# Kernel tuning notes

Hardware: AMD Instinct MI355X
Metric: run time of the kernel (lower is better)

Reference implementation:

```python
import jax, jax.numpy as jnp
import numpy as np

N_NODES = 50000
N_EDGES = 800000
F_IN = 128
HID = 32
HEADS = 8
N_CLS = 2
NEG_SLOPE = 0.2


def _segment_softmax(logits, seg, num_segments):
    # logits: [E, H], seg: [E] destination indices
    m = jax.ops.segment_max(logits, seg, num_segments=num_segments)  # [N, H]
    m = jnp.where(jnp.isfinite(m), m, 0.0)
    e = jnp.exp(logits - m[seg])
    s = jax.ops.segment_sum(e, seg, num_segments=num_segments)  # [N, H]
    return e / (s[seg] + 1e-16)


def _gat_conv(x, src, dst, W, a_src, a_dst, bias, heads, out_ch, concat):
    N = x.shape[0]
    h = (x @ W).reshape(N, heads, out_ch)           # [N, H, C]
    alpha_src = jnp.einsum('nhc,hc->nh', h, a_src)  # [N, H]
    alpha_dst = jnp.einsum('nhc,hc->nh', h, a_dst)  # [N, H]
    logits = jax.nn.leaky_relu(alpha_src[src] + alpha_dst[dst], NEG_SLOPE)  # [E, H]
    alpha = _segment_softmax(logits, dst, N)        # [E, H]
    msg = h[src] * alpha[:, :, None]                # [E, H, C]
    out = jax.ops.segment_sum(msg, dst, num_segments=N)  # [N, H, C]
    out = out.reshape(N, heads * out_ch) if concat else out.mean(axis=1)
    return out + bias


def setup_inputs() -> dict:
    key = jax.random.key(0)
    ks = jax.random.split(key, 12)
    x = jax.random.normal(ks[0], (N_NODES, F_IN), dtype=jnp.float32)
    edge_index = jax.random.randint(ks[1], (2, N_EDGES), 0, N_NODES, dtype=jnp.int32)
    batch = jnp.zeros((N_NODES,), dtype=jnp.int32)
    g1 = 1.0 / np.sqrt(F_IN)
    g2 = 1.0 / np.sqrt(HEADS * HID)
    W1 = jax.random.normal(ks[2], (F_IN, HEADS * HID), dtype=jnp.float32) * g1
    a1_src = jax.random.normal(ks[3], (HEADS, HID), dtype=jnp.float32) * g2
    a1_dst = jax.random.normal(ks[4], (HEADS, HID), dtype=jnp.float32) * g2
    b1 = jnp.zeros((HEADS * HID,), dtype=jnp.float32)
    W2 = jax.random.normal(ks[5], (HEADS * HID, N_CLS), dtype=jnp.float32) * g2
    a2_src = jax.random.normal(ks[6], (1, N_CLS), dtype=jnp.float32)
    a2_dst = jax.random.normal(ks[7], (1, N_CLS), dtype=jnp.float32)
    b2 = jnp.zeros((N_CLS,), dtype=jnp.float32)
    return {"x": x, "edge_index": edge_index, "batch": batch,
            "W1": W1, "a1_src": a1_src, "a1_dst": a1_dst, "b1": b1,
            "W2": W2, "a2_src": a2_src, "a2_dst": a2_dst, "b2": b2}


def reference(x, edge_index, batch, W1, a1_src, a1_dst, b1, W2, a2_src, a2_dst, b2):
    N = x.shape[0]
    # PyG GATConv default add_self_loops=True
    loops = jnp.arange(N, dtype=edge_index.dtype)
    src = jnp.concatenate([edge_index[0], loops])
    dst = jnp.concatenate([edge_index[1], loops])
    # dropout layers are no-ops at inference (training=False)
    h = _gat_conv(x, src, dst, W1, a1_src, a1_dst, b1, HEADS, HID, concat=True)
    h = jax.nn.elu(h)
    out = _gat_conv(h, src, dst, W2, a2_src, a2_dst, b2, 1, N_CLS, concat=False)
    return out
```

## Files before the change

### kernel.cpp

```cpp
#include <hip/hip_runtime.h>

#define NN 50000
#define NP 50048
#define NE 800000
#define ET (NE + NN)
#define NB 196
#define CAP 8192
#define EPB 4096
#define P1_B ((ET + EPB - 1) / EPB)
#define CONVW_B 32
#define CONVX_B 391
#define FRONT_B (P1_B + CONVW_B + CONVX_B)
#define GEMM_B (NP / 64)
#define MID_B (NB + GEMM_B)
#define AGG1_B 2048

typedef __attribute__((ext_vector_type(8))) short short8;
typedef __attribute__((ext_vector_type(4))) float f32x4;

static __device__ __forceinline__ float bf2f(unsigned short u) {
  union { unsigned int i; float f; } v; v.i = ((unsigned int)u) << 16; return v.f;
}
static __device__ __forceinline__ unsigned short f2bf(float f) {
  union { unsigned int i; float f; } v; v.f = f;
  unsigned int r = v.i + 0x7fffu + ((v.i >> 16) & 1u);
  return (unsigned short)(r >> 16);
}
static __device__ __forceinline__ float lrelu(float z) { return z > 0.f ? z : 0.2f * z; }

__global__ __launch_bounds__(1024) void k_front(
    const int* __restrict__ ei, int* __restrict__ gcount, int* __restrict__ tmp,
    const float* __restrict__ W1, unsigned short* __restrict__ wh,
    const float* __restrict__ x, unsigned short* __restrict__ xh) {
  __shared__ int hist[NB];
  __shared__ int lbase[NB];
  const int b = blockIdx.x;
  const int tid = threadIdx.x;
  if (b < P1_B) {
    if (tid < NB) hist[tid] = 0;
    __syncthreads();
    const int e0 = b * EPB + tid;
    int bkv[4], locv[4], pkv[4];
    bool val[4];
#pragma unroll
    for (int j = 0; j < 4; ++j) {
      int e = e0 + j * 1024;
      val[j] = (e < ET);
      int s = 0, d = 0;
      if (val[j]) {
        s = (e < NE) ? ei[e] : (e - NE);
        d = (e < NE) ? ei[NE + e] : (e - NE);
      }
      bkv[j] = d >> 8;
      pkv[j] = (s << 8) | (d & 255);
      locv[j] = val[j] ? atomicAdd(&hist[bkv[j]], 1) : 0;
    }
    __syncthreads();
    if (tid < NB) {
      int c = hist[tid];
      lbase[tid] = (c > 0) ? atomicAdd(&gcount[tid], c) : 0;
    }
    __syncthreads();
#pragma unroll
    for (int j = 0; j < 4; ++j)
      if (val[j]) tmp[bkv[j] * CAP + lbase[bkv[j]] + locv[j]] = pkv[j];
  } else if (b < P1_B + CONVW_B) {
    int i = (b - P1_B) * 1024 + tid;
    int k = i >> 8, n = i & 255;
    wh[n * 128 + k] = f2bf(W1[i]);
  } else {
    int base = (b - P1_B - CONVW_B) * 4096 + tid;
#pragma unroll
    for (int k = 0; k < 4; ++k) {
      int i4 = base + k * 1024;
      int i = i4 * 4;
      int row = i >> 7;
      float4 v = (row < NN) ? *(const float4*)(x + i) : (float4){0.f, 0.f, 0.f, 0.f};
      ushort4 h;
      h.x = f2bf(v.x);
      h.y = f2bf(v.y);
      h.z = f2bf(v.z);
      h.w = f2bf(v.w);
      *(ushort4*)(xh + i) = h;
    }
  }
}

__global__ __launch_bounds__(256) void k_mid(
    const int* __restrict__ tmp, const int* __restrict__ gcount,
    int* __restrict__ ssrc, int* __restrict__ row_ptr,
    const unsigned short* __restrict__ xh, const unsigned short* __restrict__ wh,
    const float* __restrict__ a1s, const float* __restrict__ a1d,
    unsigned short* __restrict__ h1, float* __restrict__ as1, float* __restrict__ ad1) {
  __shared__ unsigned short hst[64][264];
  const int tid = threadIdx.x;
  if (blockIdx.x < NB) {
    int* hist = (int*)&hst[0][0];
    int* sa = hist + 256;
    int* sb = sa + 256;
    int* cur = sb + 256;
    int* base_sh = cur + 256;
    const int t = tid;
    const int b = blockIdx.x;
    const int n_b = gcount[b];
    sa[t] = (t < NB) ? gcount[t] : 0;
    __syncthreads();
    {
      int* s = sa;
      int* d = sb;
      for (int off = 1; off < 256; off <<= 1) {
        int v = s[t];
        if (t >= off) v += s[t - off];
        d[t] = v;
        int* tm = s; s = d; d = tm;
        __syncthreads();
      }
      if (t == 0) {
        base_sh[0] = (b == 0) ? 0 : s[b - 1];
        if (b == 0) row_ptr[NN] = ET;
      }
    }
    hist[t] = 0;
    __syncthreads();
    const int base = base_sh[0];
    for (int i = t; i < n_b; i += 256) {
      int p = tmp[b * CAP + i];
      atomicAdd(&hist[p & 255], 1);
    }
    __syncthreads();
    sa[t] = hist[t];
    __syncthreads();
    {
      int* s = sa;
      int* d = sb;
      for (int off = 1; off < 256; off <<= 1) {
        int v = s[t];
        if (t >= off) v += s[t - off];
        d[t] = v;
        int* tm = s; s = d; d = tm;
        __syncthreads();
      }
      int excl = (t == 0) ? 0 : s[t - 1];
      int start = base + excl;
      cur[t] = start;
      int d_glob = (b << 8) + t;
      if (d_glob < NN) row_ptr[d_glob] = start;
    }
    __syncthreads();
    for (int i = t; i < n_b; i += 256) {
      int p = tmp[b * CAP + i];
      int pos = atomicAdd(&cur[p & 255], 1);
      ssrc[pos] = p >> 8;
    }
    return;
  }
  const int gb = blockIdx.x - NB;
  const int w = tid >> 6, lane = tid & 63;
  const int quad = lane >> 4, m16 = lane & 15;
  const int row0 = gb * 64;
  const int koff = quad * 8;

  f32x4 acc[4][4];
  for (int mt = 0; mt < 4; ++mt)
    for (int nt = 0; nt < 4; ++nt) acc[mt][nt] = (f32x4){0.f, 0.f, 0.f, 0.f};

  for (int kt = 0; kt < 4; ++kt) {
    short8 ah[4], bh[4];
    for (int mt = 0; mt < 4; ++mt) {
      size_t ra = (size_t)(row0 + mt * 16 + m16) * 128 + kt * 32 + koff;
      ah[mt] = *(const short8*)(xh + ra);
    }
    for (int nt = 0; nt < 4; ++nt) {
      size_t rb = (size_t)(w * 64 + nt * 16 + m16) * 128 + kt * 32 + koff;
      bh[nt] = *(const short8*)(wh + rb);
    }
    for (int mt = 0; mt < 4; ++mt)
      for (int nt = 0; nt < 4; ++nt)
        acc[mt][nt] = __builtin_amdgcn_mfma_f32_16x16x32_bf16(ah[mt], bh[nt], acc[mt][nt], 0, 0, 0);
  }
  for (int mt = 0; mt < 4; ++mt)
    for (int nt = 0; nt < 4; ++nt) {
      int c = w * 64 + nt * 16 + m16;
      int rb = mt * 16 + quad * 4;
      for (int r = 0; r < 4; ++r) hst[rb + r][c] = f2bf(acc[mt][nt][r]);
    }
  __syncthreads();
  for (int p = 0; p < 8; ++p) {
    int idx = p * 256 + tid;
    int row = idx >> 5, u4 = idx & 31;
    int grow = row0 + row;
    if (grow < NN) {
      uint4 v = *(const uint4*)&hst[row][u4 * 8];
      *(uint4*)(h1 + (size_t)grow * 256 + u4 * 8) = v;
    }
  }
  for (int p = 0; p < 2; ++p) {
    int id = p * 256 + tid;
    int row = id >> 3, head = id & 7;
    int grow = row0 + row;
    if (grow < NN) {
      float sa = 0.f, sd = 0.f;
      for (int c = 0; c < 32; ++c) {
        float hv = bf2f(hst[row][head * 32 + c]);
        sa = fmaf(hv, a1s[head * 32 + c], sa);
        sd = fmaf(hv, a1d[head * 32 + c], sd);
      }
      as1[(size_t)grow * 8 + head] = sa;
      ad1[(size_t)grow * 8 + head] = sd;
    }
  }
}

__global__ __launch_bounds__(256) void k_agg1(
    const int* __restrict__ row_ptr, const int* __restrict__ ssrc,
    const unsigned short* __restrict__ h1, const float* __restrict__ as1,
    const float* __restrict__ ad1, const float* __restrict__ b1,
    const float* __restrict__ W2, const float* __restrict__ a2s,
    const float* __restrict__ a2d, float4* __restrict__ nd) {
  const int lane = threadIdx.x & 63;
  const int hA = lane & 7;
  const int eoff = lane >> 3;
  const int hB = lane >> 3;
  const int cB = (lane & 7) * 4;
  for (int dst = (int)(blockIdx.x * 4 + (threadIdx.x >> 6)); dst < NN; dst += AGG1_B * 4) {
    const int start = row_ptr[dst], end = row_ptr[dst + 1];
    const float ad_h = ad1[(size_t)dst * 8 + hA];
    float s_loc = 0.f;
    float acc0 = 0.f, acc1 = 0.f, acc2 = 0.f, acc3 = 0.f;
    for (int base = start; base < end; base += 16) {
      int ea = base + eoff, eb = base + 8 + eoff;
      int sa_ = 0, sb_ = 0;
      float wa = 0.f, wb = 0.f;
      if (ea < end) {
        sa_ = ssrc[ea];
        wa = __expf(lrelu(as1[(size_t)sa_ * 8 + hA] + ad_h));
      }
      if (eb < end) {
        sb_ = ssrc[eb];
        wb = __expf(lrelu(as1[(size_t)sb_ * 8 + hA] + ad_h));
      }
      s_loc += wa + wb;
      uint2 u[16];
      float w16[16];
#pragma unroll
      for (int j = 0; j < 8; ++j) {
        int se = __shfl(sa_, j * 8);
        w16[j] = __shfl(wa, j * 8 + hB);
        u[j] = *(const uint2*)(h1 + (size_t)se * 256 + hB * 32 + cB);
      }
#pragma unroll
      for (int j = 0; j < 8; ++j) {
        int se = __shfl(sb_, j * 8);
        w16[8 + j] = __shfl(wb, j * 8 + hB);
        u[8 + j] = *(const uint2*)(h1 + (size_t)se * 256 + hB * 32 + cB);
      }
#pragma unroll
      for (int j = 0; j < 16; ++j) {
        float w = w16[j];
        acc0 = fmaf(w, bf2f((unsigned short)(u[j].x & 0xffffu)), acc0);
        acc1 = fmaf(w, bf2f((unsigned short)(u[j].x >> 16)), acc1);
        acc2 = fmaf(w, bf2f((unsigned short)(u[j].y & 0xffffu)), acc2);
        acc3 = fmaf(w, bf2f((unsigned short)(u[j].y >> 16)), acc3);
      }
    }
    float s_red = s_loc;
    s_red += __shfl_xor(s_red, 8);
    s_red += __shfl_xor(s_red, 16);
    s_red += __shfl_xor(s_red, 32);
    const float inv_s = 1.f / (s_red + 1e-16f);
    const float inv_sB = __shfl(inv_s, hB);
    float a0 = acc0 * inv_sB, a1 = acc1 * inv_sB, a2 = acc2 * inv_sB, a3 = acc3 * inv_sB;
    const int col = hB * 32 + cB;
    float av[4] = {a0, a1, a2, a3};
    float tp0 = 0.f, tp1 = 0.f;
    for (int j = 0; j < 4; ++j) {
      float v = av[j] + b1[col + j];
      v = v > 0.f ? v : (__expf(v) - 1.f);
      tp0 = fmaf(v, W2[(col + j) * 2 + 0], tp0);
      tp1 = fmaf(v, W2[(col + j) * 2 + 1], tp1);
    }
    for (int off = 32; off >= 1; off >>= 1) {
      tp0 += __shfl_xor(tp0, off);
      tp1 += __shfl_xor(tp1, off);
    }
    if (lane == 0) {
      float s2v = tp0 * a2s[0] + tp1 * a2s[1];
      float d2v = tp0 * a2d[0] + tp1 * a2d[1];
      nd[dst] = (float4){tp0, tp1, s2v, d2v};
    }
  }
}

__global__ __launch_bounds__(256) void k_agg2(
    const int* __restrict__ row_ptr, const int* __restrict__ ssrc,
    const float4* __restrict__ nd, const float* __restrict__ b2,
    float* __restrict__ out) {
  int gid = blockIdx.x * 256 + threadIdx.x;
  int n = gid >> 3;
  int l8 = threadIdx.x & 7;
  if (n >= NN) return;
  int st = row_ptr[n], en = row_ptr[n + 1];
  float dv = nd[n].w;
  float ssum = 0.f, o0 = 0.f, o1 = 0.f;
  for (int e = st + l8; e < en; e += 8) {
    int s = ssrc[e];
    float4 v = nd[s];
    float w = __expf(lrelu(v.z + dv));
    ssum += w;
    o0 = fmaf(w, v.x, o0);
    o1 = fmaf(w, v.y, o1);
  }
  ssum += __shfl_xor(ssum, 1); o0 += __shfl_xor(o0, 1); o1 += __shfl_xor(o1, 1);
  ssum += __shfl_xor(ssum, 2); o0 += __shfl_xor(o0, 2); o1 += __shfl_xor(o1, 2);
  ssum += __shfl_xor(ssum, 4); o0 += __shfl_xor(o0, 4); o1 += __shfl_xor(o1, 4);
  if (l8 == 0) {
    float inv = 1.f / (ssum + 1e-16f);
    out[(size_t)n * 2 + 0] = o0 * inv + b2[0];
    out[(size_t)n * 2 + 1] = o1 * inv + b2[1];
  }
}

extern "C" void kernel_launch(void* const* d_in, const int* in_sizes, int n_in,
                              void* d_out, int out_size, void* d_ws, size_t ws_size,
                              hipStream_t stream) {
  const float* x = (const float*)d_in[0];
  const int* ei = (const int*)d_in[1];
  const float* W1 = (const float*)d_in[3];
  const float* a1s = (const float*)d_in[4];
  const float* a1d = (const float*)d_in[5];
  const float* b1 = (const float*)d_in[6];
  const float* W2 = (const float*)d_in[7];
  const float* a2s = (const float*)d_in[8];
  const float* a2d = (const float*)d_in[9];
  const float* b2 = (const float*)d_in[10];
  float* out = (float*)d_out;

  char* ws = (char*)d_ws;
  size_t off = 0;
  auto alloc = [&](size_t bytes) -> void* {
    void* p = ws + off;
    off += (bytes + 255) & ~(size_t)255;
    return p;
  };
  int* gcount = (int*)alloc((size_t)NB * 4);
  int* tmp = (int*)alloc((size_t)NB * CAP * 4);
  int* row_ptr = (int*)alloc((size_t)(NN + 1) * 4);
  int* ssrc = (int*)alloc((size_t)ET * 4);
  unsigned short* xh = (unsigned short*)alloc((size_t)NP * 128 * 2);
  unsigned short* wh = (unsigned short*)alloc((size_t)32768 * 2);
  unsigned short* h1 = (unsigned short*)alloc((size_t)NN * 256 * 2);
  float* as1 = (float*)alloc((size_t)NN * 8 * 4);
  float* ad1 = (float*)alloc((size_t)NN * 8 * 4);
  float4* nd = (float4*)alloc((size_t)NN * 16);
  (void)ws_size; (void)in_sizes; (void)n_in; (void)out_size;

  hipMemsetAsync(gcount, 0, (size_t)NB * 4, stream);
  k_front<<<FRONT_B, 1024, 0, stream>>>(ei, gcount, tmp, W1, wh, x, xh);
  k_mid<<<MID_B, 256, 0, stream>>>(tmp, gcount, ssrc, row_ptr, xh, wh, a1s, a1d, h1, as1, ad1);
  k_agg1<<<AGG1_B, 256, 0, stream>>>(row_ptr, ssrc, h1, as1, ad1, b1, W2, a2s, a2d, nd);
  k_agg2<<<(NN * 8 + 255) / 256, 256, 0, stream>>>(row_ptr, ssrc, nd, b2, out);
}
```

Measured before the change: 213.8 us.

## Fuse all stages into one persistent kernel with global grid barriers

Replaces the four kernel launches with a single persistent kernel whose grid is sized from the occupancy query. Blocks loop over virtual work items in each phase and synchronize through an atomic global barrier, removing launch gaps and kernel-boundary drains. Work granularity shrinks to fit 256-thread blocks (GEMM tiles drop to 32 rows). The spin barrier relies on every block being co-resident and adds atomic polling cost at three phase boundaries.

```diff
diff --git a/kernel.cpp b/kernel.cpp
--- a/kernel.cpp
+++ b/kernel.cpp
@@ -6,14 +6,16 @@
 #define ET (NE + NN)
 #define NB 196
 #define CAP 8192
-#define EPB 4096
-#define P1_B ((ET + EPB - 1) / EPB)
-#define CONVW_B 32
-#define CONVX_B 391
-#define FRONT_B (P1_B + CONVW_B + CONVX_B)
-#define GEMM_B (NP / 64)
-#define MID_B (NB + GEMM_B)
-#define AGG1_B 2048
+
+#define P1V 831
+#define CWV 128
+#define CXV 1564
+#define PH1 (P1V + CWV + CXV)
+#define SORTV NB
+#define GEMMV 1564
+#define PH2 (SORTV + GEMMV)
+#define PH3 12500
+#define PH4 1563
 
 typedef __attribute__((ext_vector_type(8))) short short8;
 typedef __attribute__((ext_vector_type(4))) float f32x4;
@@ -28,295 +30,304 @@
 }
 static __device__ __forceinline__ float lrelu(float z) { return z > 0.f ? z : 0.2f * z; }
 
-__global__ __launch_bounds__(1024) void k_front(
-    const int* __restrict__ ei, int* __restrict__ gcount, int* __restrict__ tmp,
-    const float* __restrict__ W1, unsigned short* __restrict__ wh,
-    const float* __restrict__ x, unsigned short* __restrict__ xh) {
-  __shared__ int hist[NB];
-  __shared__ int lbase[NB];
-  const int b = blockIdx.x;
+static __device__ __forceinline__ void gbar(int* bar, int target) {
+  __syncthreads();
+  if (threadIdx.x == 0) {
+    __threadfence();
+    __hip_atomic_fetch_add(bar, 1, __ATOMIC_ACQ_REL, __HIP_MEMORY_SCOPE_AGENT);
+    while (__hip_atomic_load(bar, __ATOMIC_ACQUIRE, __HIP_MEMORY_SCOPE_AGENT) < target)
+      __builtin_amdgcn_s_sleep(2);
+    __threadfence();
+  }
+  __syncthreads();
+}
+
+__global__ __launch_bounds__(256) void k_fused(
+    int* __restrict__ bar, const int* __restrict__ ei, int* __restrict__ gcount,
+    int* __restrict__ tmp, const float* __restrict__ W1, unsigned short* __restrict__ wh,
+    const float* __restrict__ x, unsigned short* __restrict__ xh,
+    const float* __restrict__ a1s, const float* __restrict__ a1d,
+    int* __restrict__ ssrc, int* __restrict__ row_ptr,
+    unsigned short* __restrict__ h1, float* __restrict__ as1, float* __restrict__ ad1,
+    const float* __restrict__ b1, const float* __restrict__ W2,
+    const float* __restrict__ a2s, const float* __restrict__ a2d,
+    float4* __restrict__ nd, const float* __restrict__ b2, float* __restrict__ out) {
+  __shared__ __align__(16) char smraw[32 * 264 * 2];
   const int tid = threadIdx.x;
-  if (b < P1_B) {
-    if (tid < NB) hist[tid] = 0;
-    __syncthreads();
-    const int e0 = b * EPB + tid;
-    int bkv[4], locv[4], pkv[4];
-    bool val[4];
-#pragma unroll
-    for (int j = 0; j < 4; ++j) {
-      int e = e0 + j * 1024;
-      val[j] = (e < ET);
-      int s = 0, d = 0;
-      if (val[j]) {
-        s = (e < NE) ? ei[e] : (e - NE);
-        d = (e < NE) ? ei[NE + e] : (e - NE);
-      }
-      bkv[j] = d >> 8;
-      pkv[j] = (s << 8) | (d & 255);
-      locv[j] = val[j] ? atomicAdd(&hist[bkv[j]], 1) : 0;
+  const int G = (int)gridDim.x;
+
+  for (int v = blockIdx.x; v < PH1; v += G) {
+    if (v < P1V) {
+      int* hist = (int*)smraw;
+      int* lbase = hist + 256;
+      if (tid < NB) hist[tid] = 0;
+      __syncthreads();
+      int bkv[4], locv[4], pkv[4];
+      bool val[4];
+#pragma unroll
+      for (int j = 0; j < 4; ++j) {
+        int e = v * 1024 + tid + j * 256;
+        val[j] = (e < ET);
+        int s = 0, d = 0;
+        if (val[j]) {
+          s = (e < NE) ? ei[e] : (e - NE);
+          d = (e < NE) ? ei[NE + e] : (e - NE);
+        }
+        bkv[j] = d >> 8;
+        pkv[j] = (s << 8) | (d & 255);
+        locv[j] = val[j] ? atomicAdd(&hist[bkv[j]], 1) : 0;
+      }
+      __syncthreads();
+      if (tid < NB) {
+        int c = hist[tid];
+        lbase[tid] = (c > 0) ? atomicAdd(&gcount[tid], c) : 0;
+      }
+      __syncthreads();
+#pragma unroll
+      for (int j = 0; j < 4; ++j)
+        if (val[j]) tmp[bkv[j] * CAP + lbase[bkv[j]] + locv[j]] = pkv[j];
+      __syncthreads();
+    } else if (v < P1V + CWV) {
+      int i = (v - P1V) * 256 + tid;
+      int k = i >> 8, n = i & 255;
+      wh[n * 128 + k] = f2bf(W1[i]);
+    } else {
+      int base = (v - P1V - CWV) * 1024 + tid;
+#pragma unroll
+      for (int j = 0; j < 4; ++j) {
+        int i4 = base + j * 256;
+        int i = i4 * 4;
+        int row = i >> 7;
+        float4 vv = (row < NN) ? *(const float4*)(x + i) : (float4){0.f, 0.f, 0.f, 0.f};
+        ushort4 h;
+        h.x = f2bf(vv.x); h.y = f2bf(vv.y); h.z = f2bf(vv.z); h.w = f2bf(vv.w);
+        *(ushort4*)(xh + i) = h;
+      }
     }
-    __syncthreads();
-    if (tid < NB) {
-      int c = hist[tid];
-      lbase[tid] = (c > 0) ? atomicAdd(&gcount[tid], c) : 0;
+  }
+  gbar(bar, 1 * G);
+
+  for (int v = blockIdx.x; v < PH2; v += G) {
+    if (v < SORTV) {
+      int* hist = (int*)smraw;
+      int* sa = hist + 256;
+      int* sb = sa + 256;
+      int* cur = sb + 256;
+      int* base_sh = cur + 256;
+      const int t = tid;
+      const int b = v;
+      const int n_b = gcount[b];
+      sa[t] = (t < NB) ? gcount[t] : 0;
+      __syncthreads();
+      {
+        int* s = sa; int* d = sb;
+        for (int off = 1; off < 256; off <<= 1) {
+          int val = s[t];
+          if (t >= off) val += s[t - off];
+          d[t] = val;
+          int* tm = s; s = d; d = tm;
+          __syncthreads();
+        }
+        if (t == 0) {
+          base_sh[0] = (b == 0) ? 0 : s[b - 1];
+          if (b == 0) row_ptr[NN] = ET;
+        }
+      }
+      hist[t] = 0;
+      __syncthreads();
+      const int base = base_sh[0];
+      for (int i = t; i < n_b; i += 256) {
+        int p = tmp[b * CAP + i];
+        atomicAdd(&hist[p & 255], 1);
+      }
+      __syncthreads();
+      sa[t] = hist[t];
+      __syncthreads();
+      {
+        int* s = sa; int* d = sb;
+        for (int off = 1; off < 256; off <<= 1) {
+          int val = s[t];
+          if (t >= off) val += s[t - off];
+          d[t] = val;
+          int* tm = s; s = d; d = tm;
+          __syncthreads();
+        }
+        int excl = (t == 0) ? 0 : s[t - 1];
+        int start = base + excl;
+        cur[t] = start;
+        int d_glob = (b << 8) + t;
+        if (d_glob < NN) row_ptr[d_glob] = start;
+      }
+      __syncthreads();
+      for (int i = t; i < n_b; i += 256) {
+        int p = tmp[b * CAP + i];
+        int pos = atomicAdd(&cur[p & 255], 1);
+        ssrc[pos] = p >> 8;
+      }
+      __syncthreads();
+    } else {
+      unsigned short(*hst)[264] = (unsigned short(*)[264])smraw;
+      const int gv = v - SORTV;
+      const int w = tid >> 6, lane = tid & 63;
+      const int quad = lane >> 4, m16 = lane & 15;
+      const int row0 = gv * 32;
+      const int koff = quad * 8;
+      f32x4 acc[2][4];
+      for (int mt = 0; mt < 2; ++mt)
+        for (int nt = 0; nt < 4; ++nt) acc[mt][nt] = (f32x4){0.f, 0.f, 0.f, 0.f};
+      for (int kt = 0; kt < 4; ++kt) {
+        short8 ah[2], bh[4];
+        for (int mt = 0; mt < 2; ++mt) {
+          size_t ra = (size_t)(row0 + mt * 16 + m16) * 128 + kt * 32 + koff;
+          ah[mt] = *(const short8*)(xh + ra);
+        }
+        for (int nt = 0; nt < 4; ++nt) {
+          size_t rb = (size_t)(w * 64 + nt * 16 + m16) * 128 + kt * 32 + koff;
+          bh[nt] = *(const short8*)(wh + rb);
+        }
+        for (int mt = 0; mt < 2; ++mt)
+          for (int nt = 0; nt < 4; ++nt)
+            acc[mt][nt] = __builtin_amdgcn_mfma_f32_16x16x32_bf16(ah[mt], bh[nt], acc[mt][nt], 0, 0, 0);
+      }
+      for (int mt = 0; mt < 2; ++mt)
+        for (int nt = 0; nt < 4; ++nt) {
+          int c = w * 64 + nt * 16 + m16;
+          int rb = mt * 16 + quad * 4;
+          for (int r = 0; r < 4; ++r) hst[rb + r][c] = f2bf(acc[mt][nt][r]);
+        }
+      __syncthreads();
+      for (int p = 0; p < 4; ++p) {
+        int idx = p * 256 + tid;
+        int row = idx >> 5, u4 = idx & 31;
+        int grow = row0 + row;
+        if (grow < NN) {
+          uint4 vv = *(const uint4*)&hst[row][u4 * 8];
+          *(uint4*)(h1 + (size_t)grow * 256 + u4 * 8) = vv;
+        }
+      }
+      {
+        int row = tid >> 3, head = tid & 7;
+        int grow = row0 + row;
+        if (grow < NN) {
+          float sa = 0.f, sd = 0.f;
+          for (int c = 0; c < 32; ++c) {
+            float hv = bf2f(hst[row][head * 32 + c]);
+            sa = fmaf(hv, a1s[head * 32 + c], sa);
+            sd = fmaf(hv, a1d[head * 32 + c], sd);
+          }
+          as1[(size_t)grow * 8 + head] = sa;
+          ad1[(size_t)grow * 8 + head] = sd;
+        }
+      }
+      __syncthreads();
     }
-    __syncthreads();
-#pragma unroll
-    for (int j = 0; j < 4; ++j)
-      if (val[j]) tmp[bkv[j] * CAP + lbase[bkv[j]] + locv[j]] = pkv[j];
-  } else if (b < P1_B + CONVW_B) {
-    int i = (b - P1_B) * 1024 + tid;
-    int k = i >> 8, n = i & 255;
-    wh[n * 128 + k] = f2bf(W1[i]);
-  } else {
-    int base = (b - P1_B - CONVW_B) * 4096 + tid;
-#pragma unroll
-    for (int k = 0; k < 4; ++k) {
-      int i4 = base + k * 1024;
-      int i = i4 * 4;
-      int row = i >> 7;
-      float4 v = (row < NN) ? *(const float4*)(x + i) : (float4){0.f, 0.f, 0.f, 0.f};
-      ushort4 h;
-      h.x = f2bf(v.x);
-      h.y = f2bf(v.y);
-      h.z = f2bf(v.z);
-      h.w = f2bf(v.w);
-      *(ushort4*)(xh + i) = h;
+  }
+  gbar(bar, 2 * G);
+
+  {
+    const int lane = tid & 63;
+    const int wid = tid >> 6;
+    const int hA = lane & 7;
+    const int eoff = lane >> 3;
+    const int hB = lane >> 3;
+    const int cB = (lane & 7) * 4;
+    for (int v = blockIdx.x; v < PH3; v += G) {
+      const int dst = v * 4 + wid;
+      const int start = row_ptr[dst], end = row_ptr[dst + 1];
+      const float ad_h = ad1[(size_t)dst * 8 + hA];
+      float s_loc = 0.f;
+      float acc0 = 0.f, acc1 = 0.f, acc2 = 0.f, acc3 = 0.f;
+      for (int base = start; base < end; base += 16) {
+        int ea = base + eoff, eb = base + 8 + eoff;
+        int sa_ = 0, sb_ = 0;
+        float wa = 0.f, wb = 0.f;
+        if (ea < end) {
+          sa_ = ssrc[ea];
+          wa = __expf(lrelu(as1[(size_t)sa_ * 8 + hA] + ad_h));
+        }
+        if (eb < end) {
+          sb_ = ssrc[eb];
+          wb = __expf(lrelu(as1[(size_t)sb_ * 8 + hA] + ad_h));
+        }
+        s_loc += wa + wb;
+        uint2 u[16];
+        float w16[16];
+#pragma unroll
+        for (int j = 0; j < 8; ++j) {
+          int se = __shfl(sa_, j * 8);
+          w16[j] = __shfl(wa, j * 8 + hB);
+          u[j] = *(const uint2*)(h1 + (size_t)se * 256 + hB * 32 + cB);
+        }
+#pragma unroll
+        for (int j = 0; j < 8; ++j) {
+          int se = __shfl(sb_, j * 8);
+          w16[8 + j] = __shfl(wb, j * 8 + hB);
+          u[8 + j] = *(const uint2*)(h1 + (size_t)se * 256 + hB * 32 + cB);
+        }
+#pragma unroll
+        for (int j = 0; j < 16; ++j) {
+          float w = w16[j];
+          acc0 = fmaf(w, bf2f((unsigned short)(u[j].x & 0xffffu)), acc0);
+          acc1 = fmaf(w, bf2f((unsigned short)(u[j].x >> 16)), acc1);
+          acc2 = fmaf(w, bf2f((unsigned short)(u[j].y & 0xffffu)), acc2);
+          acc3 = fmaf(w, bf2f((unsigned short)(u[j].y >> 16)), acc3);
+        }
+      }
+      float s_red = s_loc;
+      s_red += __shfl_xor(s_red, 8);
+      s_red += __shfl_xor(s_red, 16);
+      s_red += __shfl_xor(s_red, 32);
+      const float inv_s = 1.f / (s_red + 1e-16f);
+      const float inv_sB = __shfl(inv_s, hB);
+      float a0 = acc0 * inv_sB, a1 = acc1 * inv_sB, a2 = acc2 * inv_sB, a3 = acc3 * inv_sB;
+      const int col = hB * 32 + cB;
+      float av[4] = {a0, a1, a2, a3};
+      float tp0 = 0.f, tp1 = 0.f;
+      for (int j = 0; j < 4; ++j) {
+        float vv = av[j] + b1[col + j];
+        vv = vv > 0.f ? vv : (__expf(vv) - 1.f);
+        tp0 = fmaf(vv, W2[(col + j) * 2 + 0], tp0);
+        tp1 = fmaf(vv, W2[(col + j) * 2 + 1], tp1);
+      }
+      for (int off = 32; off >= 1; off >>= 1) {
+        tp0 += __shfl_xor(tp0, off);
+        tp1 += __shfl_xor(tp1, off);
+      }
+      if (lane == 0) {
+        float s2v = tp0 * a2s[0] + tp1 * a2s[1];
+        float d2v = tp0 * a2d[0] + tp1 * a2d[1];
+        nd[dst] = (float4){tp0, tp1, s2v, d2v};
+      }
     }
   }
-}
-
-__global__ __launch_bounds__(256) void k_mid(
-    const int* __restrict__ tmp, const int* __restrict__ gcount,
-    int* __restrict__ ssrc, int* __restrict__ row_ptr,
-    const unsigned short* __restrict__ xh, const unsigned short* __restrict__ wh,
-    const float* __restrict__ a1s, const float* __restrict__ a1d,
-    unsigned short* __restrict__ h1, float* __restrict__ as1, float* __restrict__ ad1) {
-  __shared__ unsigned short hst[64][264];
-  const int tid = threadIdx.x;
-  if (blockIdx.x < NB) {
-    int* hist = (int*)&hst[0][0];
-    int* sa = hist + 256;
-    int* sb = sa + 256;
-    int* cur = sb + 256;
-    int* base_sh = cur + 256;
-    const int t = tid;
-    const int b = blockIdx.x;
-    const int n_b = gcount[b];
-    sa[t] = (t < NB) ? gcount[t] : 0;
-    __syncthreads();
-    {
-      int* s = sa;
-      int* d = sb;
-      for (int off = 1; off < 256; off <<= 1) {
-        int v = s[t];
-        if (t >= off) v += s[t - off];
-        d[t] = v;
-        int* tm = s; s = d; d = tm;
-        __syncthreads();
-      }
-      if (t == 0) {
-        base_sh[0] = (b == 0) ? 0 : s[b - 1];
-        if (b == 0) row_ptr[NN] = ET;
+  gbar(bar, 3 * G);
+
+  {
+    const int l8 = tid & 7;
+    for (int v = blockIdx.x; v < PH4; v += G) {
+      int n = (v * 256 + tid) >> 3;
+      if (n < NN) {
+        int st = row_ptr[n], en = row_ptr[n + 1];
+        float dv = nd[n].w;
+        float ssum = 0.f, o0 = 0.f, o1 = 0.f;
+        for (int e = st + l8; e < en; e += 8) {
+          int s = ssrc[e];
+          float4 vv = nd[s];
+          float w = __expf(lrelu(vv.z + dv));
+          ssum += w;
+          o0 = fmaf(w, vv.x, o0);
+          o1 = fmaf(w, vv.y, o1);
+        }
+        ssum += __shfl_xor(ssum, 1); o0 += __shfl_xor(o0, 1); o1 += __shfl_xor(o1, 1);
+        ssum += __shfl_xor(ssum, 2); o0 += __shfl_xor(o0, 2); o1 += __shfl_xor(o1, 2);
+        ssum += __shfl_xor(ssum, 4); o0 += __shfl_xor(o0, 4); o1 += __shfl_xor(o1, 4);
+        if (l8 == 0) {
+          float inv = 1.f / (ssum + 1e-16f);
+          out[(size_t)n * 2 + 0] = o0 * inv + b2[0];
+          out[(size_t)n * 2 + 1] = o1 * inv + b2[1];
+        }
       }
     }
-    hist[t] = 0;
-    __syncthreads();
-    const int base = base_sh[0];
-    for (int i = t; i < n_b; i += 256) {
-      int p = tmp[b * CAP + i];
-      atomicAdd(&hist[p & 255], 1);
-    }
-    __syncthreads();
-    sa[t] = hist[t];
-    __syncthreads();
-    {
-      int* s = sa;
-      int* d = sb;
-      for (int off = 1; off < 256; off <<= 1) {
-        int v = s[t];
-        if (t >= off) v += s[t - off];
-        d[t] = v;
-        int* tm = s; s = d; d = tm;
-        __syncthreads();
-      }
-      int excl = (t == 0) ? 0 : s[t - 1];
-      int start = base + excl;
-      cur[t] = start;
-      int d_glob = (b << 8) + t;
-      if (d_glob < NN) row_ptr[d_glob] = start;
-    }
-    __syncthreads();
-    for (int i = t; i < n_b; i += 256) {
-      int p = tmp[b * CAP + i];
-      int pos = atomicAdd(&cur[p & 255], 1);
-      ssrc[pos] = p >> 8;
-    }
-    return;
-  }
-  const int gb = blockIdx.x - NB;
-  const int w = tid >> 6, lane = tid & 63;
-  const int quad = lane >> 4, m16 = lane & 15;
-  const int row0 = gb * 64;
-  const int koff = quad * 8;
-
-  f32x4 acc[4][4];
-  for (int mt = 0; mt < 4; ++mt)
-    for (int nt = 0; nt < 4; ++nt) acc[mt][nt] = (f32x4){0.f, 0.f, 0.f, 0.f};
-
-  for (int kt = 0; kt < 4; ++kt) {
-    short8 ah[4], bh[4];
-    for (int mt = 0; mt < 4; ++mt) {
-      size_t ra = (size_t)(row0 + mt * 16 + m16) * 128 + kt * 32 + koff;
-      ah[mt] = *(const short8*)(xh + ra);
-    }
-    for (int nt = 0; nt < 4; ++nt) {
-      size_t rb = (size_t)(w * 64 + nt * 16 + m16) * 128 + kt * 32 + koff;
-      bh[nt] = *(const short8*)(wh + rb);
-    }
-    for (int mt = 0; mt < 4; ++mt)
-      for (int nt = 0; nt < 4; ++nt)
-        acc[mt][nt] = __builtin_amdgcn_mfma_f32_16x16x32_bf16(ah[mt], bh[nt], acc[mt][nt], 0, 0, 0);
-  }
-  for (int mt = 0; mt < 4; ++mt)
-    for (int nt = 0; nt < 4; ++nt) {
-      int c = w * 64 + nt * 16 + m16;
-      int rb = mt * 16 + quad * 4;
-      for (int r = 0; r < 4; ++r) hst[rb + r][c] = f2bf(acc[mt][nt][r]);
-    }
-  __syncthreads();
-  for (int p = 0; p < 8; ++p) {
-    int idx = p * 256 + tid;
-    int row = idx >> 5, u4 = idx & 31;
-    int grow = row0 + row;
-    if (grow < NN) {
-      uint4 v = *(const uint4*)&hst[row][u4 * 8];
-      *(uint4*)(h1 + (size_t)grow * 256 + u4 * 8) = v;
-    }
-  }
-  for (int p = 0; p < 2; ++p) {
-    int id = p * 256 + tid;
-    int row = id >> 3, head = id & 7;
-    int grow = row0 + row;
-    if (grow < NN) {
-      float sa = 0.f, sd = 0.f;
-      for (int c = 0; c < 32; ++c) {
-        float hv = bf2f(hst[row][head * 32 + c]);
-        sa = fmaf(hv, a1s[head * 32 + c], sa);
-        sd = fmaf(hv, a1d[head * 32 + c], sd);
-      }
-      as1[(size_t)grow * 8 + head] = sa;
-      ad1[(size_t)grow * 8 + head] = sd;
-    }
-  }
-}
-
-__global__ __launch_bounds__(256) void k_agg1(
-    const int* __restrict__ row_ptr, const int* __restrict__ ssrc,
-    const unsigned short* __restrict__ h1, const float* __restrict__ as1,
-    const float* __restrict__ ad1, const float* __restrict__ b1,
-    const float* __restrict__ W2, const float* __restrict__ a2s,
-    const float* __restrict__ a2d, float4* __restrict__ nd) {
-  const int lane = threadIdx.x & 63;
-  const int hA = lane & 7;
-  const int eoff = lane >> 3;
-  const int hB = lane >> 3;
-  const int cB = (lane & 7) * 4;
-  for (int dst = (int)(blockIdx.x * 4 + (threadIdx.x >> 6)); dst < NN; dst += AGG1_B * 4) {
-    const int start = row_ptr[dst], end = row_ptr[dst + 1];
-    const float ad_h = ad1[(size_t)dst * 8 + hA];
-    float s_loc = 0.f;
-    float acc0 = 0.f, acc1 = 0.f, acc2 = 0.f, acc3 = 0.f;
-    for (int base = start; base < end; base += 16) {
-      int ea = base + eoff, eb = base + 8 + eoff;
-      int sa_ = 0, sb_ = 0;
-      float wa = 0.f, wb = 0.f;
-      if (ea < end) {
-        sa_ = ssrc[ea];
-        wa = __expf(lrelu(as1[(size_t)sa_ * 8 + hA] + ad_h));
-      }
-      if (eb < end) {
-        sb_ = ssrc[eb];
-        wb = __expf(lrelu(as1[(size_t)sb_ * 8 + hA] + ad_h));
-      }
-      s_loc += wa + wb;
-      uint2 u[16];
-      float w16[16];
-#pragma unroll
-      for (int j = 0; j < 8; ++j) {
-        int se = __shfl(sa_, j * 8);
-        w16[j] = __shfl(wa, j * 8 + hB);
-        u[j] = *(const uint2*)(h1 + (size_t)se * 256 + hB * 32 + cB);
-      }
-#pragma unroll
-      for (int j = 0; j < 8; ++j) {
-        int se = __shfl(sb_, j * 8);
-        w16[8 + j] = __shfl(wb, j * 8 + hB);
-        u[8 + j] = *(const uint2*)(h1 + (size_t)se * 256 + hB * 32 + cB);
-      }
-#pragma unroll
-      for (int j = 0; j < 16; ++j) {
-        float w = w16[j];
-        acc0 = fmaf(w, bf2f((unsigned short)(u[j].x & 0xffffu)), acc0);
-        acc1 = fmaf(w, bf2f((unsigned short)(u[j].x >> 16)), acc1);
-        acc2 = fmaf(w, bf2f((unsigned short)(u[j].y & 0xffffu)), acc2);
-        acc3 = fmaf(w, bf2f((unsigned short)(u[j].y >> 16)), acc3);
-      }
-    }
-    float s_red = s_loc;
-    s_red += __shfl_xor(s_red, 8);
-    s_red += __shfl_xor(s_red, 16);
-    s_red += __shfl_xor(s_red, 32);
-    const float inv_s = 1.f / (s_red + 1e-16f);
-    const float inv_sB = __shfl(inv_s, hB);
-    float a0 = acc0 * inv_sB, a1 = acc1 * inv_sB, a2 = acc2 * inv_sB, a3 = acc3 * inv_sB;
-    const int col = hB * 32 + cB;
-    float av[4] = {a0, a1, a2, a3};
-    float tp0 = 0.f, tp1 = 0.f;
-    for (int j = 0; j < 4; ++j) {
-      float v = av[j] + b1[col + j];
-      v = v > 0.f ? v : (__expf(v) - 1.f);
-      tp0 = fmaf(v, W2[(col + j) * 2 + 0], tp0);
-      tp1 = fmaf(v, W2[(col + j) * 2 + 1], tp1);
-    }
-    for (int off = 32; off >= 1; off >>= 1) {
-      tp0 += __shfl_xor(tp0, off);
-      tp1 += __shfl_xor(tp1, off);
-    }
-    if (lane == 0) {
-      float s2v = tp0 * a2s[0] + tp1 * a2s[1];
-      float d2v = tp0 * a2d[0] + tp1 * a2d[1];
-      nd[dst] = (float4){tp0, tp1, s2v, d2v};
-    }
-  }
-}
-
-__global__ __launch_bounds__(256) void k_agg2(
-    const int* __restrict__ row_ptr, const int* __restrict__ ssrc,
-    const float4* __restrict__ nd, const float* __restrict__ b2,
-    float* __restrict__ out) {
-  int gid = blockIdx.x * 256 + threadIdx.x;
-  int n = gid >> 3;
-  int l8 = threadIdx.x & 7;
-  if (n >= NN) return;
-  int st = row_ptr[n], en = row_ptr[n + 1];
-  float dv = nd[n].w;
-  float ssum = 0.f, o0 = 0.f, o1 = 0.f;
-  for (int e = st + l8; e < en; e += 8) {
-    int s = ssrc[e];
-    float4 v = nd[s];
-    float w = __expf(lrelu(v.z + dv));
-    ssum += w;
-    o0 = fmaf(w, v.x, o0);
-    o1 = fmaf(w, v.y, o1);
-  }
-  ssum += __shfl_xor(ssum, 1); o0 += __shfl_xor(o0, 1); o1 += __shfl_xor(o1, 1);
-  ssum += __shfl_xor(ssum, 2); o0 += __shfl_xor(o0, 2); o1 += __shfl_xor(o1, 2);
-  ssum += __shfl_xor(ssum, 4); o0 += __shfl_xor(o0, 4); o1 += __shfl_xor(o1, 4);
-  if (l8 == 0) {
-    float inv = 1.f / (ssum + 1e-16f);
-    out[(size_t)n * 2 + 0] = o0 * inv + b2[0];
-    out[(size_t)n * 2 + 1] = o1 * inv + b2[1];
   }
 }
 
@@ -336,13 +347,14 @@
   float* out = (float*)d_out;
 
   char* ws = (char*)d_ws;
-  size_t off = 0;
+  int* bar = (int*)ws;
+  int* gcount = (int*)(ws + 256);
+  size_t off = 1280;
   auto alloc = [&](size_t bytes) -> void* {
     void* p = ws + off;
     off += (bytes + 255) & ~(size_t)255;
     return p;
   };
-  int* gcount = (int*)alloc((size_t)NB * 4);
   int* tmp = (int*)alloc((size_t)NB * CAP * 4);
   int* row_ptr = (int*)alloc((size_t)(NN + 1) * 4);
   int* ssrc = (int*)alloc((size_t)ET * 4);
@@ -354,9 +366,14 @@
   float4* nd = (float4*)alloc((size_t)NN * 16);
   (void)ws_size; (void)in_sizes; (void)n_in; (void)out_size;
 
-  hipMemsetAsync(gcount, 0, (size_t)NB * 4, stream);
-  k_front<<<FRONT_B, 1024, 0, stream>>>(ei, gcount, tmp, W1, wh, x, xh);
-  k_mid<<<MID_B, 256, 0, stream>>>(tmp, gcount, ssrc, row_ptr, xh, wh, a1s, a1d, h1, as1, ad1);
-  k_agg1<<<AGG1_B, 256, 0, stream>>>(row_ptr, ssrc, h1, as1, ad1, b1, W2, a2s, a2d, nd);
-  k_agg2<<<(NN * 8 + 255) / 256, 256, 0, stream>>>(row_ptr, ssrc, nd, b2, out);
-}
+  int nb = 0;
+  if (hipOccupancyMaxActiveBlocksPerMultiprocessor(&nb, k_fused, 256, 0) != hipSuccess || nb < 1)
+    nb = 1;
+  int G = nb * 256;
+  if (G > 2048) G = 2048;
+
+  hipMemsetAsync(ws, 0, 1040, stream);
+  k_fused<<<G, 256, 0, stream>>>(bar, ei, gcount, tmp, W1, wh, x, xh, a1s, a1d,
+                                 ssrc, row_ptr, h1, as1, ad1, b1, W2, a2s, a2d,
+                                 nd, b2, out);
+}
```

Result: slower. 442.8 us (+107.1%).
